# Performance work log

Hardware: AMD Instinct MI355X
Metric: run time of the kernel (lower is better)

The kernel has to match this reference:

```python
import jax, jax.numpy as jnp
import numpy as np

EMBED_DIM = 32
PIC_RES = 96
KERNEL_BW = 3.0
STEP_SIZE = 0.5
NB_ITERS = 3


def setup_inputs() -> dict:
    key = jax.random.key(0)
    # scale down so exp(bw * x^T x) stays in a safe numeric range
    x_in = jax.random.normal(key, (1, EMBED_DIM, PIC_RES, PIC_RES), dtype=jnp.float32) * 0.1
    return {"x_in": x_in}


def reference(x_in):
    # x: [D, N], N = res*res pixels
    x = x_in.reshape(EMBED_DIM, -1)
    outs = []
    for _ in range(NB_ITERS):
        # affinity K[i,j] = exp(bw * <x_i, x_j>), shape [N, N]
        K = jnp.exp(KERNEL_BW * (x.T @ x))
        # column sums d_j = sum_i K[i,j] (== torch diag(K^T @ 1)); K is symmetric
        d = K.sum(axis=0)
        # x <- x @ (step * K diag(1/d) + (1-step) I)
        x = STEP_SIZE * (x @ K) / d + (1.0 - STEP_SIZE) * x
        outs.append(x.reshape(EMBED_DIM, PIC_RES, PIC_RES))
    final = x.reshape(EMBED_DIM, PIC_RES, PIC_RES)
    return final, jnp.stack(outs)
```

## Files before the change

### kernel.cpp

```cpp
#include <hip/hip_runtime.h>
#include <hip/hip_bf16.h>
#include <math.h>


#define D 32
#define NPIX 9216
#define NSPLIT 16
#define JB 256
#define NJB (NPIX / JB)
#define IPB (NPIX / NSPLIT)
#define ICH 64
#define XST 56
#define TS  40

typedef __attribute__((ext_vector_type(8))) short short8;
typedef __attribute__((ext_vector_type(4))) short short4v;
typedef __attribute__((ext_vector_type(4))) float f32x4;

#if __has_builtin(__builtin_amdgcn_exp2f)
#define EXP2F __builtin_amdgcn_exp2f
#else
#define EXP2F exp2f
#endif

#define C3 4.32808512266689f

__device__ __forceinline__ unsigned pack2_bf16(float a, float b) {
    union { __hip_bfloat162 h2; unsigned u; } c;
    c.h2 = __float22bfloat162_rn(make_float2(a, b));
    return c.u;
}
__device__ __forceinline__ short pack1_bf16(float a) {
    union { __hip_bfloat16 h; unsigned short s; } c;
    c.h = __float2bfloat16(a);
    return (short)c.s;
}

__global__ __launch_bounds__(256, 2) void accum_kernel(
    const short* __restrict__ xb,
    const short* __restrict__ xbT,
    float* __restrict__ num_part,
    float* __restrict__ den_part)
{
    __shared__ __align__(16) short xiT_s[2][32 * XST];
    __shared__ __align__(16) short xi_s [2][32 * XST];

    const int t = threadIdx.x;
    const int wid = t >> 6, lane = t & 63, quad = lane >> 4, m = lane & 15;
    const int bj = blockIdx.x % NJB, bi = blockIdx.x / NJB;
    const int j0 = bj * JB + wid * 64;
    const int i0b = bi * IPB;

    short8 bfrag[4];
#pragma unroll
    for (int jt = 0; jt < 4; ++jt)
        bfrag[jt] = *(const short8*)&xbT[(size_t)(j0 + jt * 16 + m) * D + quad * 8];

    f32x4 acc[2][4] = {};
    float dacc[4] = {0.f, 0.f, 0.f, 0.f};

    const int srT = t >> 2, hT = srT >> 5, ilT = srT & 31, cT = (t & 3) * 8;
    const int sgm = ((ilT & 4) << 2) + ((ilT >> 3) << 2) + (ilT & 3);
    const int dV = t >> 3, cV = (t & 7) >> 2, qV = (t & 3) * 8;

    for (int ic = 0; ic < IPB; ic += ICH) {
        const int i0 = i0b + ic;
        __syncthreads();
        *(short8*)&xiT_s[hT][sgm * XST + cT] =
            *(const short8*)&xbT[(size_t)(i0 + srT) * D + cT];
        *(short8*)&xi_s[cV][dV * XST + qV] =
            *(const short8*)&xb[dV * NPIX + i0 + cV * 32 + qV];
        __syncthreads();

#pragma unroll
        for (int h = 0; h < 2; ++h) {
            short8 aT0 = *(const short8*)&xiT_s[h][m * XST + quad * 8];
            short8 aT1 = *(const short8*)&xiT_s[h][(16 + m) * XST + quad * 8];
            short8 aV0 = *(const short8*)&xi_s[h][m * XST + quad * 8];
            short8 aV1 = *(const short8*)&xi_s[h][(16 + m) * XST + quad * 8];

#pragma unroll
            for (int jt = 0; jt < 4; ++jt) {
                f32x4 z = {0.f, 0.f, 0.f, 0.f};
                f32x4 s0 = __builtin_amdgcn_mfma_f32_16x16x32_bf16(aT0, bfrag[jt], z, 0, 0, 0);
                f32x4 s1 = __builtin_amdgcn_mfma_f32_16x16x32_bf16(aT1, bfrag[jt], z, 0, 0, 0);

                float w[8];
#pragma unroll
                for (int r = 0; r < 4; ++r) { w[r]     = EXP2F(C3 * s0[r]);
                                              w[4 + r] = EXP2F(C3 * s1[r]); }
#pragma unroll
                for (int r = 0; r < 8; ++r) dacc[jt] += w[r];

                union { short8 s; unsigned u[4]; } wb;
                wb.u[0] = pack2_bf16(w[0], w[1]);
                wb.u[1] = pack2_bf16(w[2], w[3]);
                wb.u[2] = pack2_bf16(w[4], w[5]);
                wb.u[3] = pack2_bf16(w[6], w[7]);

                acc[0][jt] = __builtin_amdgcn_mfma_f32_16x16x32_bf16(aV0, wb.s, acc[0][jt], 0, 0, 0);
                acc[1][jt] = __builtin_amdgcn_mfma_f32_16x16x32_bf16(aV1, wb.s, acc[1][jt], 0, 0, 0);
            }
        }
    }

    float* np = num_part + (size_t)bi * D * NPIX;
#pragma unroll
    for (int dt = 0; dt < 2; ++dt)
#pragma unroll
        for (int jt = 0; jt < 4; ++jt)
#pragma unroll
            for (int r = 0; r < 4; ++r)
                np[(dt * 16 + quad * 4 + r) * NPIX + j0 + jt * 16 + m] = acc[dt][jt][r];
#pragma unroll
    for (int jt = 0; jt < 4; ++jt) {
        float v = dacc[jt];
        v += __shfl_xor(v, 16, 64);
        v += __shfl_xor(v, 32, 64);
        if (quad == 0) den_part[bi * NPIX + j0 + jt * 16 + m] = v;
    }
}

__global__ __launch_bounds__(256) void combine_kernel(
    const float* __restrict__ xin,
    const float* __restrict__ num_part, const float* __restrict__ den_part,
    float* __restrict__ xout, float* __restrict__ xfinal,
    short* __restrict__ xb, short* __restrict__ xbT, int do_ms)
{
    __shared__ __align__(16) short tile[32 * TS];
    const int t = threadIdx.x;
    const int il = t & 31, q = t >> 5;
    const int i = blockIdx.x * 32 + il;
    const int d0 = q * 4;

    float inv = 0.f;
    if (do_ms) {
        float den = 0.f;
#pragma unroll
        for (int s = 0; s < NSPLIT; ++s) den += den_part[s * NPIX + i];
        inv = 0.5f / den;
    }

#pragma unroll
    for (int dd = 0; dd < 4; ++dd) {
        const int d = d0 + dd;
        const int idx = d * NPIX + i;
        float v;
        if (do_ms) {
            float nm = 0.f;
#pragma unroll
            for (int s = 0; s < NSPLIT; ++s) nm += num_part[(s * D + d) * NPIX + i];
            v = nm * inv + 0.5f * xin[idx];
            xout[idx] = v;
            if (xfinal) xfinal[idx] = v;
        } else {
            v = xin[idx];
        }
        short b = pack1_bf16(v);
        xb[idx] = b;
        tile[il * TS + d] = b;
    }
    __syncthreads();
    const int i2 = t >> 3, dc = (t & 7) * 4;
    *(short4v*)&xbT[(blockIdx.x * 32 + i2) * D + dc] =
        *(const short4v*)&tile[i2 * TS + dc];
}

extern "C" void kernel_launch(void* const* d_in, const int* in_sizes, int n_in,
                              void* d_out, int out_size, void* d_ws, size_t ws_size,
                              hipStream_t stream)
{
    const float* x0 = (const float*)d_in[0];
    float* out = (float*)d_out;
    const size_t slot = (size_t)D * NPIX;

    float* num_part = (float*)d_ws;
    float* den_part = num_part + (size_t)NSPLIT * slot;
    short* xb  = (short*)(den_part + (size_t)NSPLIT * NPIX);
    short* xbT = xb + slot;

    combine_kernel<<<dim3(NPIX / 32), dim3(256), 0, stream>>>(
        x0, nullptr, nullptr, nullptr, nullptr, xb, xbT, 0);

    for (int t = 0; t < 3; ++t) {
        accum_kernel<<<dim3(NJB * NSPLIT), dim3(256), 0, stream>>>(
            xb, xbT, num_part, den_part);
        const float* xin = (t == 0) ? x0 : (out + (size_t)t * slot);
        combine_kernel<<<dim3(NPIX / 32), dim3(256), 0, stream>>>(
            xin, num_part, den_part, out + (size_t)(t + 1) * slot,
            (t == 2) ? out : nullptr, xb, xbT, 1);
    }
}
```

Baseline: 173.8 us.

## Triple-buffer LDS via direct global_load_lds and compute denominators with MFMA

Replaces the register-staged, double-synchronized LDS fill with asynchronous global-to-LDS loads into a three-stage ring buffer. Each chunk now needs a single barrier and the next chunk's load overlaps compute. The per-column denominator is computed by an extra MFMA against a ones vector instead of scalar adds and shuffles. Split count rises to 24 and occupancy target to 3 blocks/SM, which adds more partial sums for the combine step to reduce. Denominators now sum bf16-rounded weights, a small accuracy change.

```diff
diff --git a/kernel.cpp b/kernel.cpp
--- a/kernel.cpp
+++ b/kernel.cpp
@@ -5,12 +5,12 @@
 
 #define D 32
 #define NPIX 9216
-#define NSPLIT 16
+#define NSPLIT 24
 #define JB 256
 #define NJB (NPIX / JB)
 #define IPB (NPIX / NSPLIT)
 #define ICH 64
-#define XST 56
+#define NCH (IPB / ICH)
 #define TS  40
 
 typedef __attribute__((ext_vector_type(8))) short short8;
@@ -36,14 +36,20 @@
     return (short)c.s;
 }
 
-__global__ __launch_bounds__(256, 2) void accum_kernel(
+__device__ __forceinline__ void gll16(const void* g, void* l) {
+    __builtin_amdgcn_global_load_lds(
+        (const __attribute__((address_space(1))) void*)g,
+        (__attribute__((address_space(3))) void*)l, 16, 0, 0);
+}
+
+__global__ __launch_bounds__(256, 3) void accum_kernel(
     const short* __restrict__ xb,
     const short* __restrict__ xbT,
     float* __restrict__ num_part,
     float* __restrict__ den_part)
 {
-    __shared__ __align__(16) short xiT_s[2][32 * XST];
-    __shared__ __align__(16) short xi_s [2][32 * XST];
+    __shared__ __align__(16) short sT[3][2048];
+    __shared__ __align__(16) short sV[3][2048];
 
     const int t = threadIdx.x;
     const int wid = t >> 6, lane = t & 63, quad = lane >> 4, m = lane & 15;
@@ -56,28 +62,45 @@
     for (int jt = 0; jt < 4; ++jt)
         bfrag[jt] = *(const short8*)&xbT[(size_t)(j0 + jt * 16 + m) * D + quad * 8];
 
+    short8 ones;
+#pragma unroll
+    for (int e = 0; e < 8; ++e) ones[e] = (short)0x3F80;
+
     f32x4 acc[2][4] = {};
-    float dacc[4] = {0.f, 0.f, 0.f, 0.f};
-
-    const int srT = t >> 2, hT = srT >> 5, ilT = srT & 31, cT = (t & 3) * 8;
-    const int sgm = ((ilT & 4) << 2) + ((ilT >> 3) << 2) + (ilT & 3);
-    const int dV = t >> 3, cV = (t & 7) >> 2, qV = (t & 3) * 8;
-
-    for (int ic = 0; ic < IPB; ic += ICH) {
-        const int i0 = i0b + ic;
-        __syncthreads();
-        *(short8*)&xiT_s[hT][sgm * XST + cT] =
-            *(const short8*)&xbT[(size_t)(i0 + srT) * D + cT];
-        *(short8*)&xi_s[cV][dV * XST + qV] =
-            *(const short8*)&xb[dV * NPIX + i0 + cV * 32 + qV];
-        __syncthreads();
-
+    f32x4 accden[4] = {};
+
+    const int ch = t >> 7, cq = (t >> 5) & 3, ci = t & 31;
+    const int invi = (((ci >> 3) & 1) << 4) | (((ci >> 2) & 1) << 3)
+                   | (((ci >> 4) & 1) << 2) | (ci & 3);
+    const short* srcT = xbT + (size_t)(i0b + ch * 32 + invi) * D + cq * 8;
+    const short* srcV = xb + (size_t)ci * NPIX + i0b + ch * 32 + cq * 8;
+    short* dT = &sT[0][0] + wid * 512;
+    short* dV = &sV[0][0] + wid * 512;
+
+    gll16(srcT, dT);
+    gll16(srcV, dV);
+
+#pragma unroll
+    for (int n = 0; n < NCH; ++n) {
+        if (n + 1 < NCH) {
+            gll16(srcT + (size_t)(n + 1) * (ICH * D), dT + ((n + 1) % 3) * 2048);
+            gll16(srcV + (n + 1) * ICH,               dV + ((n + 1) % 3) * 2048);
+            asm volatile("s_waitcnt vmcnt(2)" ::: "memory");
+        } else {
+            asm volatile("s_waitcnt vmcnt(0)" ::: "memory");
+        }
+        __builtin_amdgcn_s_barrier();
+        __builtin_amdgcn_sched_barrier(0);
+
+        const short* bT = &sT[n % 3][0];
+        const short* bV = &sV[n % 3][0];
 #pragma unroll
         for (int h = 0; h < 2; ++h) {
-            short8 aT0 = *(const short8*)&xiT_s[h][m * XST + quad * 8];
-            short8 aT1 = *(const short8*)&xiT_s[h][(16 + m) * XST + quad * 8];
-            short8 aV0 = *(const short8*)&xi_s[h][m * XST + quad * 8];
-            short8 aV1 = *(const short8*)&xi_s[h][(16 + m) * XST + quad * 8];
+            const int rb = (h * 128 + quad * 32 + m) * 8;
+            short8 aT0 = *(const short8*)&bT[rb];
+            short8 aT1 = *(const short8*)&bT[rb + 128];
+            short8 aV0 = *(const short8*)&bV[rb];
+            short8 aV1 = *(const short8*)&bV[rb + 128];
 
 #pragma unroll
             for (int jt = 0; jt < 4; ++jt) {
@@ -89,8 +112,6 @@
 #pragma unroll
                 for (int r = 0; r < 4; ++r) { w[r]     = EXP2F(C3 * s0[r]);
                                               w[4 + r] = EXP2F(C3 * s1[r]); }
-#pragma unroll
-                for (int r = 0; r < 8; ++r) dacc[jt] += w[r];
 
                 union { short8 s; unsigned u[4]; } wb;
                 wb.u[0] = pack2_bf16(w[0], w[1]);
@@ -98,6 +119,7 @@
                 wb.u[2] = pack2_bf16(w[4], w[5]);
                 wb.u[3] = pack2_bf16(w[6], w[7]);
 
+                accden[jt] = __builtin_amdgcn_mfma_f32_16x16x32_bf16(ones, wb.s, accden[jt], 0, 0, 0);
                 acc[0][jt] = __builtin_amdgcn_mfma_f32_16x16x32_bf16(aV0, wb.s, acc[0][jt], 0, 0, 0);
                 acc[1][jt] = __builtin_amdgcn_mfma_f32_16x16x32_bf16(aV1, wb.s, acc[1][jt], 0, 0, 0);
             }
@@ -113,12 +135,8 @@
             for (int r = 0; r < 4; ++r)
                 np[(dt * 16 + quad * 4 + r) * NPIX + j0 + jt * 16 + m] = acc[dt][jt][r];
 #pragma unroll
-    for (int jt = 0; jt < 4; ++jt) {
-        float v = dacc[jt];
-        v += __shfl_xor(v, 16, 64);
-        v += __shfl_xor(v, 32, 64);
-        if (quad == 0) den_part[bi * NPIX + j0 + jt * 16 + m] = v;
-    }
+    for (int jt = 0; jt < 4; ++jt)
+        if (quad == 0) den_part[bi * NPIX + j0 + jt * 16 + m] = accden[jt][0];
 }
 
 __global__ __launch_bounds__(256) void combine_kernel(
```

New measurement: 164.1 us. 5.6% less time.
